# Performance work log

Measured on AMD Instinct MI355X. Metric: run time of the kernel, lower is better.

Reference implementation:

```python
import jax, jax.numpy as jnp
import numpy as np
import math

DIM = 1024
NUM_HEADS = 16
SHARED_HEADS = 1
ROUTED_HEADS = 3
HEAD_DIM = DIM // NUM_HEADS
B, N = 2, 2048


def setup_inputs() -> dict:
    key = jax.random.key(0)
    ks = jax.random.split(key, 16)
    s = 1.0 / math.sqrt(DIM)
    inp = {
        "x": jax.random.normal(ks[0], (B, N, DIM), dtype=jnp.float32),
        "Wq": jax.random.uniform(ks[1], (DIM, DIM), minval=-s, maxval=s),
        "bq": jax.random.uniform(ks[2], (DIM,), minval=-s, maxval=s),
        "Wk": jax.random.uniform(ks[3], (DIM, DIM), minval=-s, maxval=s),
        "bk": jax.random.uniform(ks[4], (DIM,), minval=-s, maxval=s),
        "Wv": jax.random.uniform(ks[5], (DIM, DIM), minval=-s, maxval=s),
        "bv": jax.random.uniform(ks[6], (DIM,), minval=-s, maxval=s),
        "Wp": jax.random.uniform(ks[7], (DIM, DIM), minval=-s, maxval=s),
        "bp": jax.random.uniform(ks[8], (DIM,), minval=-s, maxval=s),
        "Wr": jax.random.uniform(ks[9], (NUM_HEADS - SHARED_HEADS, DIM), minval=-s, maxval=s),
        "br": jax.random.uniform(ks[10], (NUM_HEADS - SHARED_HEADS,), minval=-s, maxval=s),
        "Ws": jax.random.uniform(ks[11], (2, DIM), minval=-s, maxval=s),
        "bs": jax.random.uniform(ks[12], (2,), minval=-s, maxval=s),
        # temperature init: log(exp(1/0.24)-1), shape (H,1,1)
        "temperature": jnp.full((NUM_HEADS, 1, 1), float(np.log(np.expm1(1.0 / 0.24))), dtype=jnp.float32),
        "query_embedding": 0.02 * jax.random.normal(ks[13], (NUM_HEADS, 1, HEAD_DIM), dtype=jnp.float32),
    }
    return inp


def reference(x, Wq, bq, Wk, bk, Wv, bv, Wp, bp, Wr, br, Ws, bs, temperature, query_embedding):
    Bsz, Nn, C = x.shape
    H, hd = NUM_HEADS, HEAD_DIM

    def heads(W, b):
        y = x @ W.T + b  # [B,N,C]
        return y.reshape(Bsz, Nn, H, hd).transpose(0, 2, 1, 3)  # [B,H,N,hd]

    q = heads(Wq, bq)
    k = heads(Wk, bk)
    v = heads(Wv, bv)

    q_norm = q / jnp.linalg.norm(q, axis=-1, keepdims=True)
    q_scaled = (q_norm + query_embedding[None]) * jax.nn.softplus(temperature)[None]
    attn = jnp.einsum("bhqd,bhkd->bhqk", q_scaled, k) / math.sqrt(hd)
    attn = jax.nn.softmax(attn, axis=-1)
    h = jnp.einsum("bhqk,bhkd->bhqd", attn, v)
    h = h.transpose(0, 2, 1, 3).reshape(Bsz, Nn, C)  # [B,N,C]

    # routed-head gating
    gates = jax.nn.softmax(h @ Wr.T + br, axis=-1)  # [B,N,H-shared]
    _, idx = jax.lax.top_k(gates, ROUTED_HEADS)
    # NOTE: original uses num_classes=num_heads-shared_heads for one_hot
    mask = jax.nn.one_hot(idx, H - SHARED_HEADS, dtype=gates.dtype).sum(axis=-2)
    routed_gates = gates * mask * ROUTED_HEADS

    sw = jax.nn.softmax(h @ Ws.T + bs, axis=-1)  # [B,N,2]
    shared_gates = sw * SHARED_HEADS
    weight_0 = sw * 2.0
    shared_gates = weight_0[..., 0:1] * shared_gates
    routed_gates = weight_0[..., 1:2] * routed_gates
    masked_gates = jnp.concatenate([shared_gates, routed_gates], axis=-1)

    # einsum('bnc,bnd->bnd') == per-token scalar sum over c times h
    out = h * masked_gates.sum(axis=-1, keepdims=True)
    return out @ Wp.T + bp
```

## Files before the change

### kernel.cpp

```cpp
#include <hip/hip_runtime.h>
#include <hip/hip_bf16.h>

typedef short s16x8 __attribute__((ext_vector_type(8)));
typedef float f32x4 __attribute__((ext_vector_type(4)));

__device__ __forceinline__ float b2f(unsigned short u) {
    union { unsigned int i; float f; } v;
    v.i = ((unsigned int)u) << 16;
    return v.f;
}
__device__ __forceinline__ unsigned int pkbf16(float a, float b) {
    union { __hip_bfloat162 h; unsigned int u; } v;
    v.h = __float22bfloat162_rn(make_float2(a, b));
    return v.u;
}
__device__ __forceinline__ float fast_exp2(float x) {
#if __has_builtin(__builtin_amdgcn_exp2f)
    return __builtin_amdgcn_exp2f(x);
#else
    return exp2f(x);
#endif
}

__device__ __forceinline__ void gl_lds16(const unsigned short* g, unsigned short* l) {
    __builtin_amdgcn_global_load_lds(
        (const __attribute__((address_space(1))) void*)g,
        (__attribute__((address_space(3))) void*)l, 16, 0, 0);
}


__device__ __forceinline__ void cvt8(const float* __restrict__ s,
                                     unsigned short* __restrict__ d, int i) {
    const float* p = s + (size_t)i * 8;
    float4 a = *(const float4*)p;
    float4 b = *(const float4*)(p + 4);
    unsigned int u0 = pkbf16(a.x, a.y), u1 = pkbf16(a.z, a.w);
    unsigned int u2 = pkbf16(b.x, b.y), u3 = pkbf16(b.z, b.w);
    uint4 o = {u0, u1, u2, u3};
    *(uint4*)&d[(size_t)i * 8] = o;
}

__global__ __launch_bounds__(256) void cvt_main(
    const float* __restrict__ x,  const float* __restrict__ Wq,
    const float* __restrict__ Wk, const float* __restrict__ Wv,
    const float* __restrict__ Wr, const float* __restrict__ Ws,
    const float* __restrict__ bq, const float* __restrict__ bk,
    const float* __restrict__ bv,
    unsigned short* __restrict__ xb, unsigned short* __restrict__ wqkv,
    unsigned short* __restrict__ wg, float* __restrict__ bqkv)
{
    int blk = blockIdx.x, t = threadIdx.x;
    if (blk < 2048)      cvt8(x,  xb,             blk * 256 + t);
    else if (blk < 2560) cvt8(Wq, wqkv,           (blk - 2048) * 256 + t);
    else if (blk < 3072) cvt8(Wk, wqkv + 1048576, (blk - 2560) * 256 + t);
    else if (blk < 3584) cvt8(Wv, wqkv + 2097152, (blk - 3072) * 256 + t);
    else if (blk < 3592) { int i = (blk - 3584) * 256 + t; if (i < 1920) cvt8(Wr, wg, i); }
    else if (blk < 3593) { int i = t; cvt8(Ws, wg + 15360, i); }
    else {
        int i = (blk - 3593) * 256 + t;
        bqkv[i] = (i < 1024) ? bq[i] : (i < 2048) ? bk[i - 1024] : bv[i - 2048];
    }
}

__global__ __launch_bounds__(256) void qkv_gemm(
    const unsigned short* __restrict__ A,
    const unsigned short* __restrict__ Bw,
    const float* __restrict__ bias,
    unsigned short* __restrict__ Q, unsigned short* __restrict__ K,
    unsigned short* __restrict__ Vt)
{
    __shared__ __attribute__((aligned(16))) unsigned short As[128 * 64];
    __shared__ __attribute__((aligned(16))) unsigned short Bs[128 * 64];
    const int t = threadIdx.x;
    const int wave = t >> 6, lane = t & 63;
    const int m0 = blockIdx.x * 128, n0 = blockIdx.y * 128;
    const int wm = (wave >> 1) * 64, wn = (wave & 1) * 64;
    const int lr = lane & 15, lq = lane >> 4;
    const int srow = lane >> 3;
    const int scol = (((lane & 7) ^ srow) << 3);

    f32x4 acc[4][4];
#pragma unroll
    for (int i = 0; i < 4; ++i)
#pragma unroll
        for (int j = 0; j < 4; ++j) acc[i][j] = (f32x4){0.f, 0.f, 0.f, 0.f};

    for (int k0 = 0; k0 < 1024; k0 += 64) {
        __syncthreads();
#pragma unroll
        for (int i = 0; i < 4; ++i) {
            int rb = wave * 32 + i * 8;
            gl_lds16(&A[(size_t)(m0 + rb + srow) * 1024 + k0 + scol], &As[rb * 64]);
            gl_lds16(&Bw[(size_t)(n0 + rb + srow) * 1024 + k0 + scol], &Bs[rb * 64]);
        }
        __syncthreads();
#pragma unroll
        for (int kk = 0; kk < 64; kk += 32) {
            const int po = ((((kk >> 3) + lq) ^ (lr & 7)) << 3);
            s16x8 af[4], bf[4];
#pragma unroll
            for (int i = 0; i < 4; ++i)
                af[i] = *(const s16x8*)&As[(wm + i * 16 + lr) * 64 + po];
#pragma unroll
            for (int j = 0; j < 4; ++j)
                bf[j] = *(const s16x8*)&Bs[(wn + j * 16 + lr) * 64 + po];
#pragma unroll
            for (int i = 0; i < 4; ++i)
#pragma unroll
                for (int j = 0; j < 4; ++j)
                    acc[i][j] = __builtin_amdgcn_mfma_f32_16x16x32_bf16(af[i], bf[j], acc[i][j], 0, 0, 0);
        }
    }
    const int kind = n0 >> 10;
    const int nc = n0 & 1023;
    if (kind < 2) {
        unsigned short* Cm = kind ? K : Q;
#pragma unroll
        for (int j = 0; j < 4; ++j) {
            int cl = wn + j * 16 + lr;
            float bv = bias[n0 + cl];
#pragma unroll
            for (int i = 0; i < 4; ++i) {
                int rowb = m0 + wm + i * 16 + lq * 4;
                unsigned int u0 = pkbf16(acc[i][j][0] + bv, acc[i][j][1] + bv);
                unsigned int u1 = pkbf16(acc[i][j][2] + bv, acc[i][j][3] + bv);
                Cm[(size_t)(rowb + 0) * 1024 + nc + cl] = (unsigned short)u0;
                Cm[(size_t)(rowb + 1) * 1024 + nc + cl] = (unsigned short)(u0 >> 16);
                Cm[(size_t)(rowb + 2) * 1024 + nc + cl] = (unsigned short)u1;
                Cm[(size_t)(rowb + 3) * 1024 + nc + cl] = (unsigned short)(u1 >> 16);
            }
        }
    } else {
        const int bb = m0 >> 11;
#pragma unroll
        for (int j = 0; j < 4; ++j) {
            int col = nc + wn + j * 16 + lr;
            int hh = col >> 6, dd = col & 63;
            float bv = bias[n0 + wn + j * 16 + lr];
#pragma unroll
            for (int i = 0; i < 4; ++i) {
                int tokb = m0 + wm + i * 16 + lq * 4;
                int tloc = tokb & 2047;
                uint2 u;
                u.x = pkbf16(acc[i][j][0] + bv, acc[i][j][1] + bv);
                u.y = pkbf16(acc[i][j][2] + bv, acc[i][j][3] + bv);
                *(uint2*)&Vt[((size_t)(bb * 16 + hh) * 64 + dd) * 2048 + tloc] = u;
            }
        }
    }
}

__global__ __launch_bounds__(256) void attn_kernel(
    const unsigned short* __restrict__ Q,
    const unsigned short* __restrict__ Kb,
    const unsigned short* __restrict__ Vt,
    const float* __restrict__ temp,
    const float* __restrict__ qe,
    unsigned short* __restrict__ Hout)
{
    __shared__ __attribute__((aligned(16))) unsigned short Ks[128 * 64];
    __shared__ __attribute__((aligned(16))) unsigned short Vs[64 * 128];
    __shared__ __attribute__((aligned(16))) unsigned short Ps[128 * 72];
    const int t = threadIdx.x, wave = t >> 6, lane = t & 63;
    const int lr = lane & 15, lq = lane >> 4;
    const int bh = blockIdx.x, b = bh >> 4, h = bh & 15;
    const int q0 = blockIdx.y * 128;
    const int srow = lane >> 3;
    const int scol = (((lane & 7) ^ srow) << 3);

#pragma unroll
    for (int i = 0; i < 4; ++i) {
        int rb = wave * 32 + i * 8;
        gl_lds16(&Q[(size_t)(b * 2048 + q0 + rb + srow) * 1024 + h * 64 + scol], &Ks[rb * 64]);
    }
    __syncthreads();

    float tv = temp[h];
    float sp = ((tv > 20.f) ? tv : log1pf(__expf(tv))) * 0.18033688f;
    s16x8 aq[2][2];
#pragma unroll
    for (int i = 0; i < 2; ++i) {
        float v[2][8];
        float ss = 0.f;
#pragma unroll
        for (int kk = 0; kk < 2; ++kk) {
            const int po = (((kk * 4 + lq) ^ (lr & 7)) << 3);
            s16x8 f = *(const s16x8*)&Ks[(wave * 32 + i * 16 + lr) * 64 + po];
#pragma unroll
            for (int e = 0; e < 8; ++e) {
                v[kk][e] = b2f((unsigned short)f[e]);
                ss += v[kk][e] * v[kk][e];
            }
        }
        ss += __shfl_xor(ss, 16); ss += __shfl_xor(ss, 32);
        float rn = rsqrtf(ss);
#pragma unroll
        for (int kk = 0; kk < 2; ++kk) {
            const float* qh = qe + h * 64 + kk * 32 + lq * 8;
#pragma unroll
            for (int e = 0; e < 8; e += 2) {
                unsigned int u = pkbf16((v[kk][e] * rn + qh[e]) * sp,
                                        (v[kk][e + 1] * rn + qh[e + 1]) * sp);
                aq[i][kk][e] = (short)u; aq[i][kk][e + 1] = (short)(u >> 16);
            }
        }
    }

    f32x4 accO[2][4];
#pragma unroll
    for (int i = 0; i < 2; ++i)
#pragma unroll
        for (int j = 0; j < 4; ++j) accO[i][j] = (f32x4){0.f, 0.f, 0.f, 0.f};
    float lsum[2][4] = {{0.f, 0.f, 0.f, 0.f}, {0.f, 0.f, 0.f, 0.f}};

    for (int kc = 0; kc < 2048; kc += 128) {
        __syncthreads();
#pragma unroll
        for (int i = 0; i < 4; ++i) {
            int rb = wave * 32 + i * 8;
            gl_lds16(&Kb[(size_t)(b * 2048 + kc + rb + srow) * 1024 + h * 64 + scol], &Ks[rb * 64]);
        }
#pragma unroll
        for (int i = 0; i < 4; ++i) {
            int rb = wave * 16 + i * 4;
            int vrow = rb + (lane >> 4);
            int vcb = lane & 15;
            gl_lds16(&Vt[((size_t)(b * 16 + h) * 64 + vrow) * 2048 + kc + ((vcb ^ (vrow & 7)) << 3)],
                     &Vs[rb * 128]);
        }
        __syncthreads();

#pragma unroll
        for (int hh = 0; hh < 2; ++hh) {
            const int half = hh ^ (wave & 1);
            f32x4 s[2][4];
#pragma unroll
            for (int i = 0; i < 2; ++i)
#pragma unroll
                for (int j = 0; j < 4; ++j) s[i][j] = (f32x4){0.f, 0.f, 0.f, 0.f};
#pragma unroll
            for (int kk = 0; kk < 2; ++kk) {
                const int po = (((kk * 4 + lq) ^ (lr & 7)) << 3);
                s16x8 bk[4];
#pragma unroll
                for (int j = 0; j < 4; ++j)
                    bk[j] = *(const s16x8*)&Ks[(half * 64 + j * 16 + lr) * 64 + po];
#pragma unroll
                for (int i = 0; i < 2; ++i)
#pragma unroll
                    for (int j = 0; j < 4; ++j)
                        s[i][j] = __builtin_amdgcn_mfma_f32_16x16x32_bf16(aq[i][kk], bk[j], s[i][j], 0, 0, 0);
            }

#pragma unroll
            for (int i = 0; i < 2; ++i)
#pragma unroll
                for (int r = 0; r < 4; ++r) {
                    float p0 = fast_exp2(s[i][0][r]), p1 = fast_exp2(s[i][1][r]);
                    float p2 = fast_exp2(s[i][2][r]), p3 = fast_exp2(s[i][3][r]);
                    lsum[i][r] += (p0 + p1) + (p2 + p3);
                    unsigned int ua = pkbf16(p0, p1), ub = pkbf16(p2, p3);
                    int base = (wave * 32 + i * 16 + lq * 4 + r) * 72 + lr;
                    Ps[base]      = (unsigned short)ua;
                    Ps[base + 16] = (unsigned short)(ua >> 16);
                    Ps[base + 32] = (unsigned short)ub;
                    Ps[base + 48] = (unsigned short)(ub >> 16);
                }

#pragma unroll
            for (int kk = 0; kk < 2; ++kk) {
                const int vb = (((half * 8 + kk * 4 + lq) ^ (lr & 7)) << 3);
                s16x8 ap[2], bv[4];
#pragma unroll
                for (int i = 0; i < 2; ++i)
                    ap[i] = *(const s16x8*)&Ps[(wave * 32 + i * 16 + lr) * 72 + kk * 32 + lq * 8];
#pragma unroll
                for (int j = 0; j < 4; ++j)
                    bv[j] = *(const s16x8*)&Vs[(j * 16 + lr) * 128 + vb];
#pragma unroll
                for (int i = 0; i < 2; ++i)
#pragma unroll
                    for (int j = 0; j < 4; ++j)
                        accO[i][j] = __builtin_amdgcn_mfma_f32_16x16x32_bf16(ap[i], bv[j], accO[i][j], 0, 0, 0);
            }
        }
    }

#pragma unroll
    for (int i = 0; i < 2; ++i)
#pragma unroll
        for (int r = 0; r < 4; ++r) {
            float l = lsum[i][r];
            l += __shfl_xor(l, 1); l += __shfl_xor(l, 2);
            l += __shfl_xor(l, 4); l += __shfl_xor(l, 8);
            float inv = 1.f / l;
            int row = q0 + wave * 32 + i * 16 + lq * 4 + r;
            size_t ob = (size_t)(b * 2048 + row) * 1024 + h * 64 + lr;
            unsigned int u0 = pkbf16(accO[i][0][r] * inv, accO[i][1][r] * inv);
            unsigned int u1 = pkbf16(accO[i][2][r] * inv, accO[i][3][r] * inv);
            Hout[ob]      = (unsigned short)u0;
            Hout[ob + 16] = (unsigned short)(u0 >> 16);
            Hout[ob + 32] = (unsigned short)u1;
            Hout[ob + 48] = (unsigned short)(u1 >> 16);
        }
}

__global__ __launch_bounds__(256) void gate_g(
    const unsigned short* __restrict__ Hb,
    const unsigned short* __restrict__ Wg,
    const float* __restrict__ br, const float* __restrict__ bs,
    const float* __restrict__ Wp, unsigned short* __restrict__ wpb,
    float* __restrict__ g)
{
    __shared__ __attribute__((aligned(16))) unsigned short As[4][16 * 64];
    __shared__ __attribute__((aligned(16))) unsigned short Gs[4][32 * 64];
    __shared__ float Lred[4][16][32];
    const int t = threadIdx.x, wave = t >> 6, lane = t & 63;
    const int lr = lane & 15, lq = lane >> 4;
    const int m0 = blockIdx.x * 16;
    const int srow = lane >> 3;
    const int scol = (((lane & 7) ^ srow) << 3);

    cvt8(Wp, wpb, blockIdx.x * 512 + t);
    cvt8(Wp, wpb, blockIdx.x * 512 + 256 + t);

    f32x4 acc[2];
    acc[0] = (f32x4){0.f, 0.f, 0.f, 0.f};
    acc[1] = (f32x4){0.f, 0.f, 0.f, 0.f};

    for (int k0 = wave * 64; k0 < 1024; k0 += 256) {
        gl_lds16(&Hb[(size_t)(m0 + srow) * 1024 + k0 + scol], &As[wave][0]);
        gl_lds16(&Hb[(size_t)(m0 + 8 + srow) * 1024 + k0 + scol], &As[wave][8 * 64]);
#pragma unroll
        for (int i = 0; i < 4; ++i) {
            int row = i * 8 + srow;
            int wr = (row > 16) ? 16 : row;
            gl_lds16(&Wg[(size_t)wr * 1024 + k0 + scol], &Gs[wave][i * 8 * 64]);
        }
        __syncthreads();
#pragma unroll
        for (int kk = 0; kk < 64; kk += 32) {
            const int po = ((((kk >> 3) + lq) ^ (lr & 7)) << 3);
            s16x8 af = *(const s16x8*)&As[wave][lr * 64 + po];
#pragma unroll
            for (int j = 0; j < 2; ++j) {
                s16x8 gf = *(const s16x8*)&Gs[wave][(j * 16 + lr) * 64 + po];
                acc[j] = __builtin_amdgcn_mfma_f32_16x16x32_bf16(af, gf, acc[j], 0, 0, 0);
            }
        }
    }
#pragma unroll
    for (int j = 0; j < 2; ++j)
#pragma unroll
        for (int r = 0; r < 4; ++r)
            Lred[wave][lq * 4 + r][j * 16 + lr] = acc[j][r];
    __syncthreads();
    if (t < 16) {
        float lg[17];
#pragma unroll
        for (int j = 0; j < 17; ++j)
            lg[j] = Lred[0][t][j] + Lred[1][t][j] + Lred[2][t][j] + Lred[3][t][j]
                  + ((j < 15) ? br[j] : bs[j - 15]);
        float mx = lg[0];
#pragma unroll
        for (int j = 1; j < 15; ++j) mx = fmaxf(mx, lg[j]);
        float sum = 0.f, v1 = -1.f, v2 = -1.f, v3 = -1.f;
#pragma unroll
        for (int j = 0; j < 15; ++j) {
            float e = __expf(lg[j] - mx);
            sum += e;
            if (e > v1)      { v3 = v2; v2 = v1; v1 = e; }
            else if (e > v2) { v3 = v2; v2 = e; }
            else if (e > v3) { v3 = e; }
        }
        float tops = (v1 + v2 + v3) / sum;
        float sm = fmaxf(lg[15], lg[16]);
        float e0 = __expf(lg[15] - sm), e1 = __expf(lg[16] - sm);
        float inv = 1.f / (e0 + e1);
        g[m0 + t] = 2.f * (e0 * inv) + 6.f * (e1 * inv) * tops;
    }
}

__global__ __launch_bounds__(256) void gemm64_out(
    const unsigned short* __restrict__ A,
    const unsigned short* __restrict__ Bw,
    const float* __restrict__ bias,
    const float* __restrict__ g,
    float* __restrict__ C)
{
    __shared__ __attribute__((aligned(16))) unsigned short As[64 * 64];
    __shared__ __attribute__((aligned(16))) unsigned short Bs[64 * 64];
    const int t = threadIdx.x, wave = t >> 6, lane = t & 63;
    const int lr = lane & 15, lq = lane >> 4;
    const int m0 = blockIdx.x * 64, n0 = blockIdx.y * 64;
    const int wm = (wave >> 1) * 32, wn = (wave & 1) * 32;
    const int srow = lane >> 3;
    const int scol = (((lane & 7) ^ srow) << 3);

    f32x4 acc[2][2];
#pragma unroll
    for (int i = 0; i < 2; ++i)
#pragma unroll
        for (int j = 0; j < 2; ++j) acc[i][j] = (f32x4){0.f, 0.f, 0.f, 0.f};

    for (int k0 = 0; k0 < 1024; k0 += 64) {
        __syncthreads();
#pragma unroll
        for (int i = 0; i < 2; ++i) {
            int rb = wave * 16 + i * 8;
            gl_lds16(&A[(size_t)(m0 + rb + srow) * 1024 + k0 + scol], &As[rb * 64]);
            gl_lds16(&Bw[(size_t)(n0 + rb + srow) * 1024 + k0 + scol], &Bs[rb * 64]);
        }
        __syncthreads();
#pragma unroll
        for (int kk = 0; kk < 64; kk += 32) {
            const int po = ((((kk >> 3) + lq) ^ (lr & 7)) << 3);
            s16x8 af[2], bf[2];
#pragma unroll
            for (int i = 0; i < 2; ++i)
                af[i] = *(const s16x8*)&As[(wm + i * 16 + lr) * 64 + po];
#pragma unroll
            for (int j = 0; j < 2; ++j)
                bf[j] = *(const s16x8*)&Bs[(wn + j * 16 + lr) * 64 + po];
#pragma unroll
            for (int i = 0; i < 2; ++i)
#pragma unroll
                for (int j = 0; j < 2; ++j)
                    acc[i][j] = __builtin_amdgcn_mfma_f32_16x16x32_bf16(af[i], bf[j], acc[i][j], 0, 0, 0);
        }
    }
#pragma unroll
    for (int i = 0; i < 2; ++i) {
        const float4 gi = *(const float4*)&g[m0 + wm + i * 16 + lq * 4];
        float gv[4] = {gi.x, gi.y, gi.z, gi.w};
#pragma unroll
        for (int j = 0; j < 2; ++j) {
            int col = n0 + wn + j * 16 + lr;
            float bv = bias[col];
            int rowb = m0 + wm + i * 16 + lq * 4;
#pragma unroll
            for (int r = 0; r < 4; ++r)
                C[(size_t)(rowb + r) * 1024 + col] = acc[i][j][r] * gv[r] + bv;
        }
    }
}

extern "C" void kernel_launch(void* const* d_in, const int* in_sizes, int n_in,
                              void* d_out, int out_size, void* d_ws, size_t ws_size,
                              hipStream_t stream)
{
    (void)in_sizes; (void)n_in; (void)out_size; (void)ws_size;
    const float* x   = (const float*)d_in[0];
    const float* Wq  = (const float*)d_in[1];
    const float* bq  = (const float*)d_in[2];
    const float* Wk  = (const float*)d_in[3];
    const float* bk  = (const float*)d_in[4];
    const float* Wv  = (const float*)d_in[5];
    const float* bv  = (const float*)d_in[6];
    const float* Wp  = (const float*)d_in[7];
    const float* bp  = (const float*)d_in[8];
    const float* Wr  = (const float*)d_in[9];
    const float* br  = (const float*)d_in[10];
    const float* Ws  = (const float*)d_in[11];
    const float* bs  = (const float*)d_in[12];
    const float* temperature = (const float*)d_in[13];
    const float* qe  = (const float*)d_in[14];
    float* out = (float*)d_out;

    const size_t MB = 1048576;
    unsigned short* qb   = (unsigned short*)d_ws;
    unsigned short* kb   = (unsigned short*)((char*)d_ws + 8 * MB);
    unsigned short* hb   = (unsigned short*)((char*)d_ws + 16 * MB);
    unsigned short* wqkv = (unsigned short*)((char*)d_ws + 24 * MB);
    unsigned short* wg   = (unsigned short*)((char*)d_ws + 30 * MB);
    float*          bqkv = (float*)((char*)d_ws + 30 * MB + 65536);
    float*          gbuf = (float*)((char*)d_ws + 30 * MB + 131072);
    unsigned short* xb = (unsigned short*)d_out;
    unsigned short* vt = xb + 4 * MB;
    unsigned short* wpb = qb;

    dim3 blk(256);
    cvt_main<<<dim3(3605), blk, 0, stream>>>(x, Wq, Wk, Wv, Wr, Ws, bq, bk, bv,
                                             xb, wqkv, wg, bqkv);
    qkv_gemm<<<dim3(32, 24), blk, 0, stream>>>(xb, wqkv, bqkv, qb, kb, vt);
    attn_kernel<<<dim3(32, 16), blk, 0, stream>>>(qb, kb, vt, temperature, qe, hb);
    gate_g<<<dim3(256), blk, 0, stream>>>(hb, wg, br, bs, Wp, wpb, gbuf);
    gemm64_out<<<dim3(64, 16), blk, 0, stream>>>(hb, wpb, bp, gbuf, out);
}
```

Before: 215.6 us.

## Rewrite attention with 32x32 MFMA, register-resident P, and double-buffered K/V

Restructures the attention kernel to use 32x32x16 bf16 MFMA with S computed transposed (K as A operand), so P stays in registers and is rearranged via v_permlane32_swap instead of round-tripping through LDS. K/V tiles shrink to 64 keys and are double-buffered with the next tile's global-to-LDS load issued before compute, removing one barrier per iteration. It also adds s_setprio around MFMA bursts. Risks include an uncoalesced per-element scalar output store at the end and correctness of the permlane fragment layout.

```diff
diff --git a/kernel.cpp b/kernel.cpp
--- a/kernel.cpp
+++ b/kernel.cpp
@@ -3,6 +3,7 @@
 
 typedef short s16x8 __attribute__((ext_vector_type(8)));
 typedef float f32x4 __attribute__((ext_vector_type(4)));
+typedef float f32x16 __attribute__((ext_vector_type(16)));
 
 __device__ __forceinline__ float b2f(unsigned short u) {
     union { unsigned int i; float f; } v;
@@ -28,6 +29,16 @@
         (__attribute__((address_space(3))) void*)l, 16, 0, 0);
 }
 
+__device__ __forceinline__ void perm32swap(unsigned int &a, unsigned int &b) {
+    asm("v_permlane32_swap_b32 %0, %1" : "+v"(a), "+v"(b));
+}
+
+__device__ __forceinline__ s16x8 mk8(unsigned int a, unsigned int b,
+                                     unsigned int c, unsigned int d) {
+    union { uint4 u; s16x8 h; } v;
+    v.u = make_uint4(a, b, c, d);
+    return v.h;
+}
 
 __device__ __forceinline__ void cvt8(const float* __restrict__ s,
                                      unsigned short* __restrict__ d, int i) {
@@ -158,150 +169,146 @@
     const float* __restrict__ qe,
     unsigned short* __restrict__ Hout)
 {
-    __shared__ __attribute__((aligned(16))) unsigned short Ks[128 * 64];
-    __shared__ __attribute__((aligned(16))) unsigned short Vs[64 * 128];
-    __shared__ __attribute__((aligned(16))) unsigned short Ps[128 * 72];
+    __shared__ __attribute__((aligned(16))) unsigned short Ks[2][64 * 64];
+    __shared__ __attribute__((aligned(16))) unsigned short Vs[2][64 * 64];
+    __shared__ float Lred[4][32];
     const int t = threadIdx.x, wave = t >> 6, lane = t & 63;
-    const int lr = lane & 15, lq = lane >> 4;
+    const int l31 = lane & 31, hi = lane >> 5;
     const int bh = blockIdx.x, b = bh >> 4, h = bh & 15;
     const int q0 = blockIdx.y * 128;
     const int srow = lane >> 3;
     const int scol = (((lane & 7) ^ srow) << 3);
+    unsigned short* KsF = &Ks[0][0];
+
+    auto stageK = [&](int kc, int cb) {
+#pragma unroll
+        for (int i2 = 0; i2 < 2; ++i2) {
+            int rb = wave * 16 + i2 * 8;
+            gl_lds16(&Kb[(size_t)(b * 2048 + kc + rb + srow) * 1024 + h * 64 + scol],
+                     &Ks[cb][rb * 64]);
+        }
+    };
+    auto stageV = [&](int kc, int cb) {
+#pragma unroll
+        for (int i2 = 0; i2 < 2; ++i2) {
+            int rb = wave * 16 + i2 * 8;
+            gl_lds16(&Vt[((size_t)(b * 16 + h) * 64 + rb + srow) * 2048 + kc + scol],
+                     &Vs[cb][rb * 64]);
+        }
+    };
 
 #pragma unroll
     for (int i = 0; i < 4; ++i) {
         int rb = wave * 32 + i * 8;
-        gl_lds16(&Q[(size_t)(b * 2048 + q0 + rb + srow) * 1024 + h * 64 + scol], &Ks[rb * 64]);
+        gl_lds16(&Q[(size_t)(b * 2048 + q0 + rb + srow) * 1024 + h * 64 + scol],
+                 &KsF[rb * 64]);
     }
     __syncthreads();
+
+    s16x8 qf[4];
+#pragma unroll
+    for (int kd = 0; kd < 4; ++kd)
+        qf[kd] = *(const s16x8*)&KsF[(wave * 32 + l31) * 64 + (((kd * 2 + hi) ^ (l31 & 7)) << 3)];
+    __syncthreads();
+
+    stageK(0, 0);
+    stageV(0, 0);
 
     float tv = temp[h];
     float sp = ((tv > 20.f) ? tv : log1pf(__expf(tv))) * 0.18033688f;
-    s16x8 aq[2][2];
-#pragma unroll
-    for (int i = 0; i < 2; ++i) {
-        float v[2][8];
+    s16x8 aqB[4];
+    {
+        float v[4][8];
         float ss = 0.f;
 #pragma unroll
-        for (int kk = 0; kk < 2; ++kk) {
-            const int po = (((kk * 4 + lq) ^ (lr & 7)) << 3);
-            s16x8 f = *(const s16x8*)&Ks[(wave * 32 + i * 16 + lr) * 64 + po];
+        for (int kd = 0; kd < 4; ++kd)
 #pragma unroll
             for (int e = 0; e < 8; ++e) {
-                v[kk][e] = b2f((unsigned short)f[e]);
-                ss += v[kk][e] * v[kk][e];
+                v[kd][e] = b2f((unsigned short)qf[kd][e]);
+                ss += v[kd][e] * v[kd][e];
             }
-        }
-        ss += __shfl_xor(ss, 16); ss += __shfl_xor(ss, 32);
+        ss += __shfl_xor(ss, 32);
         float rn = rsqrtf(ss);
 #pragma unroll
-        for (int kk = 0; kk < 2; ++kk) {
-            const float* qh = qe + h * 64 + kk * 32 + lq * 8;
-#pragma unroll
-            for (int e = 0; e < 8; e += 2) {
-                unsigned int u = pkbf16((v[kk][e] * rn + qh[e]) * sp,
-                                        (v[kk][e + 1] * rn + qh[e + 1]) * sp);
-                aq[i][kk][e] = (short)u; aq[i][kk][e + 1] = (short)(u >> 16);
+        for (int kd = 0; kd < 4; ++kd) {
+            const float* qh = qe + h * 64 + kd * 16 + hi * 8;
+            unsigned int w0 = pkbf16((v[kd][0] * rn + qh[0]) * sp, (v[kd][1] * rn + qh[1]) * sp);
+            unsigned int w1 = pkbf16((v[kd][2] * rn + qh[2]) * sp, (v[kd][3] * rn + qh[3]) * sp);
+            unsigned int w2 = pkbf16((v[kd][4] * rn + qh[4]) * sp, (v[kd][5] * rn + qh[5]) * sp);
+            unsigned int w3 = pkbf16((v[kd][6] * rn + qh[6]) * sp, (v[kd][7] * rn + qh[7]) * sp);
+            aqB[kd] = mk8(w0, w1, w2, w3);
+        }
+    }
+
+    f32x16 accO[2];
+#pragma unroll
+    for (int r = 0; r < 16; ++r) { accO[0][r] = 0.f; accO[1][r] = 0.f; }
+    float lsum = 0.f;
+
+    for (int it = 0; it < 32; ++it) {
+        const int c = it & 1;
+        __syncthreads();
+        if (it < 31) { stageK((it + 1) * 64, c ^ 1); stageV((it + 1) * 64, c ^ 1); }
+
+#pragma unroll
+        for (int jj = 0; jj < 2; ++jj) {
+            const int j = jj ^ (wave & 1);
+
+            s16x8 kf[4];
+#pragma unroll
+            for (int kd = 0; kd < 4; ++kd)
+                kf[kd] = *(const s16x8*)&Ks[c][(j * 32 + l31) * 64 + (((kd * 2 + hi) ^ (l31 & 7)) << 3)];
+            f32x16 s;
+#pragma unroll
+            for (int r = 0; r < 16; ++r) s[r] = 0.f;
+            __builtin_amdgcn_s_setprio(1);
+#pragma unroll
+            for (int kd = 0; kd < 4; ++kd)
+                s = __builtin_amdgcn_mfma_f32_32x32x16_bf16(kf[kd], aqB[kd], s, 0, 0, 0);
+            __builtin_amdgcn_s_setprio(0);
+
+            float p[16];
+#pragma unroll
+            for (int r = 0; r < 16; ++r) p[r] = fast_exp2(s[r]);
+            lsum += (((p[0] + p[1]) + (p[2] + p[3])) + ((p[4] + p[5]) + (p[6] + p[7])))
+                  + (((p[8] + p[9]) + (p[10] + p[11])) + ((p[12] + p[13]) + (p[14] + p[15])));
+            unsigned int u[8];
+#pragma unroll
+            for (int g = 0; g < 8; ++g) u[g] = pkbf16(p[2 * g], p[2 * g + 1]);
+
+#pragma unroll
+            for (int kh = 0; kh < 2; ++kh) {
+                unsigned int a0 = u[4 * kh + 0], b0 = u[4 * kh + 2];
+                unsigned int a1 = u[4 * kh + 1], b1 = u[4 * kh + 3];
+                perm32swap(a0, b0);
+                perm32swap(a1, b1);
+                s16x8 pf = mk8(a0, a1, b0, b1);
+                const int vb = (((j * 4 + kh * 2 + hi) ^ (l31 & 7)) << 3);
+                s16x8 v0 = *(const s16x8*)&Vs[c][(l31) * 64 + vb];
+                s16x8 v1 = *(const s16x8*)&Vs[c][(32 + l31) * 64 + vb];
+                __builtin_amdgcn_s_setprio(1);
+                accO[0] = __builtin_amdgcn_mfma_f32_32x32x16_bf16(pf, v0, accO[0], 0, 0, 0);
+                accO[1] = __builtin_amdgcn_mfma_f32_32x32x16_bf16(pf, v1, accO[1], 0, 0, 0);
+                __builtin_amdgcn_s_setprio(0);
             }
         }
     }
 
-    f32x4 accO[2][4];
-#pragma unroll
-    for (int i = 0; i < 2; ++i)
-#pragma unroll
-        for (int j = 0; j < 4; ++j) accO[i][j] = (f32x4){0.f, 0.f, 0.f, 0.f};
-    float lsum[2][4] = {{0.f, 0.f, 0.f, 0.f}, {0.f, 0.f, 0.f, 0.f}};
-
-    for (int kc = 0; kc < 2048; kc += 128) {
-        __syncthreads();
-#pragma unroll
-        for (int i = 0; i < 4; ++i) {
-            int rb = wave * 32 + i * 8;
-            gl_lds16(&Kb[(size_t)(b * 2048 + kc + rb + srow) * 1024 + h * 64 + scol], &Ks[rb * 64]);
-        }
-#pragma unroll
-        for (int i = 0; i < 4; ++i) {
-            int rb = wave * 16 + i * 4;
-            int vrow = rb + (lane >> 4);
-            int vcb = lane & 15;
-            gl_lds16(&Vt[((size_t)(b * 16 + h) * 64 + vrow) * 2048 + kc + ((vcb ^ (vrow & 7)) << 3)],
-                     &Vs[rb * 128]);
-        }
-        __syncthreads();
-
-#pragma unroll
-        for (int hh = 0; hh < 2; ++hh) {
-            const int half = hh ^ (wave & 1);
-            f32x4 s[2][4];
-#pragma unroll
-            for (int i = 0; i < 2; ++i)
-#pragma unroll
-                for (int j = 0; j < 4; ++j) s[i][j] = (f32x4){0.f, 0.f, 0.f, 0.f};
-#pragma unroll
-            for (int kk = 0; kk < 2; ++kk) {
-                const int po = (((kk * 4 + lq) ^ (lr & 7)) << 3);
-                s16x8 bk[4];
-#pragma unroll
-                for (int j = 0; j < 4; ++j)
-                    bk[j] = *(const s16x8*)&Ks[(half * 64 + j * 16 + lr) * 64 + po];
-#pragma unroll
-                for (int i = 0; i < 2; ++i)
-#pragma unroll
-                    for (int j = 0; j < 4; ++j)
-                        s[i][j] = __builtin_amdgcn_mfma_f32_16x16x32_bf16(aq[i][kk], bk[j], s[i][j], 0, 0, 0);
-            }
-
-#pragma unroll
-            for (int i = 0; i < 2; ++i)
-#pragma unroll
-                for (int r = 0; r < 4; ++r) {
-                    float p0 = fast_exp2(s[i][0][r]), p1 = fast_exp2(s[i][1][r]);
-                    float p2 = fast_exp2(s[i][2][r]), p3 = fast_exp2(s[i][3][r]);
-                    lsum[i][r] += (p0 + p1) + (p2 + p3);
-                    unsigned int ua = pkbf16(p0, p1), ub = pkbf16(p2, p3);
-                    int base = (wave * 32 + i * 16 + lq * 4 + r) * 72 + lr;
-                    Ps[base]      = (unsigned short)ua;
-                    Ps[base + 16] = (unsigned short)(ua >> 16);
-                    Ps[base + 32] = (unsigned short)ub;
-                    Ps[base + 48] = (unsigned short)(ub >> 16);
-                }
-
-#pragma unroll
-            for (int kk = 0; kk < 2; ++kk) {
-                const int vb = (((half * 8 + kk * 4 + lq) ^ (lr & 7)) << 3);
-                s16x8 ap[2], bv[4];
-#pragma unroll
-                for (int i = 0; i < 2; ++i)
-                    ap[i] = *(const s16x8*)&Ps[(wave * 32 + i * 16 + lr) * 72 + kk * 32 + lq * 8];
-#pragma unroll
-                for (int j = 0; j < 4; ++j)
-                    bv[j] = *(const s16x8*)&Vs[(j * 16 + lr) * 128 + vb];
-#pragma unroll
-                for (int i = 0; i < 2; ++i)
-#pragma unroll
-                    for (int j = 0; j < 4; ++j)
-                        accO[i][j] = __builtin_amdgcn_mfma_f32_16x16x32_bf16(ap[i], bv[j], accO[i][j], 0, 0, 0);
-            }
-        }
-    }
-
-#pragma unroll
-    for (int i = 0; i < 2; ++i)
-#pragma unroll
-        for (int r = 0; r < 4; ++r) {
-            float l = lsum[i][r];
-            l += __shfl_xor(l, 1); l += __shfl_xor(l, 2);
-            l += __shfl_xor(l, 4); l += __shfl_xor(l, 8);
-            float inv = 1.f / l;
-            int row = q0 + wave * 32 + i * 16 + lq * 4 + r;
-            size_t ob = (size_t)(b * 2048 + row) * 1024 + h * 64 + lr;
-            unsigned int u0 = pkbf16(accO[i][0][r] * inv, accO[i][1][r] * inv);
-            unsigned int u1 = pkbf16(accO[i][2][r] * inv, accO[i][3][r] * inv);
-            Hout[ob]      = (unsigned short)u0;
-            Hout[ob + 16] = (unsigned short)(u0 >> 16);
-            Hout[ob + 32] = (unsigned short)u1;
-            Hout[ob + 48] = (unsigned short)(u1 >> 16);
+    lsum += __shfl_xor(lsum, 32);
+    if (hi == 0) Lred[wave][l31] = 1.f / lsum;
+    __syncthreads();
+    float invv[16];
+#pragma unroll
+    for (int r = 0; r < 16; ++r)
+        invv[r] = Lred[wave][(r & 3) + 8 * (r >> 2) + 4 * hi];
+#pragma unroll
+    for (int jd = 0; jd < 2; ++jd)
+#pragma unroll
+        for (int r = 0; r < 16; ++r) {
+            int qrow = (r & 3) + 8 * (r >> 2) + 4 * hi;
+            float val = accO[jd][r] * invv[r];
+            Hout[(size_t)(b * 2048 + q0 + wave * 32 + qrow) * 1024 + h * 64 + jd * 32 + l31] =
+                (unsigned short)pkbf16(val, val);
         }
 }
 
```

New measurement: 215.8 us. No clear change (+0.1%).
